# Kernel optimization log

Hardware: AMD Instinct MI355X
Metric: run time of the kernel (lower is better)

Reference implementation:

```python
import jax, jax.numpy as jnp
import numpy as np

D_MODEL = 1024
N_HEADS = 16
SCALES = (1, 2, 4, 8)
B, S = 4, 2048
NS = len(SCALES)
E = D_MODEL // NS        # per-scale embed dim = 256
H = N_HEADS // NS        # per-scale heads = 4
DK = E // H              # head dim = 64


def setup_inputs() -> dict:
    key = jax.random.key(0)
    ks = jax.random.split(key, 6)
    sc = lambda fan_in: 1.0 / np.sqrt(fan_in)
    return {
        "x": jax.random.normal(ks[0], (B, S, D_MODEL), jnp.float32),
        # per-scale projection Linear(d_model -> E), stacked over scales
        "proj_W": jax.random.normal(ks[1], (NS, D_MODEL, E), jnp.float32) * sc(D_MODEL),
        "proj_b": jnp.zeros((NS, E), jnp.float32),
        # per-scale MultiheadAttention in_proj (q,k,v packed) and out_proj
        "in_W": jax.random.normal(ks[2], (NS, E, 3 * E), jnp.float32) * sc(E),
        "in_b": jnp.zeros((NS, 3 * E), jnp.float32),
        "out_W": jax.random.normal(ks[3], (NS, E, E), jnp.float32) * sc(E),
        "out_b": jnp.zeros((NS, E), jnp.float32),
        # fusion: Linear(d_model -> d_model) + LayerNorm (dropout is identity in eval)
        "fus_W": jax.random.normal(ks[4], (D_MODEL, D_MODEL), jnp.float32) * sc(D_MODEL),
        "fus_b": jnp.zeros((D_MODEL,), jnp.float32),
        "ln_g": jnp.ones((D_MODEL,), jnp.float32),
        "ln_b": jnp.zeros((D_MODEL,), jnp.float32),
    }


def _mha(x, in_W, in_b, out_W, out_b):
    # torch nn.MultiheadAttention, batch_first, eval mode, need_weights=True
    b, L, _ = x.shape
    qkv = x @ in_W + in_b                       # [b, L, 3E]
    q, k, v = jnp.split(qkv, 3, axis=-1)
    heads = lambda t: t.reshape(b, L, H, DK).transpose(0, 2, 1, 3)  # [b,h,L,dk]
    q, k, v = heads(q), heads(k), heads(v)
    scores = jnp.einsum('bhqd,bhkd->bhqk', q, k) / np.sqrt(DK).astype(np.float32)
    probs = jax.nn.softmax(scores, axis=-1)
    o = jnp.einsum('bhqk,bhkd->bhqd', probs, v).transpose(0, 2, 1, 3).reshape(b, L, E)
    return o @ out_W + out_b, probs.mean(axis=1)  # averaged over heads: [b,L,L]


def _upsample(y, s):
    # Faithful vectorization of the torch interpolation loop when S % s == 0:
    # full[k*s + j] = (1 - j/s)*y[k] + (j/s)*y[k+1], with zero right-neighbor
    # for the last block (torch reads attn_out_full[S-1] while it is still 0).
    if s == 1:
        return y
    b, K, d = y.shape
    y_next = jnp.concatenate([y[:, 1:], jnp.zeros_like(y[:, :1])], axis=1)
    alpha = (jnp.arange(s, dtype=y.dtype) / s)[None, None, :, None]  # [1,1,s,1]
    full = (1.0 - alpha) * y[:, :, None, :] + alpha * y_next[:, :, None, :]
    return full.reshape(b, K * s, d)


def reference(x, proj_W, proj_b, in_W, in_b, out_W, out_b, fus_W, fus_b, ln_g, ln_b):
    scale_outputs = []
    w0 = None
    for i, s in enumerate(SCALES):
        x_scale = x @ proj_W[i] + proj_b[i]        # [B,S,E]
        x_sub = x_scale[:, ::s, :]                 # strided subsequence [B,S//s,E]
        y, w = _mha(x_sub, in_W[i], in_b[i], out_W[i], out_b[i])
        scale_outputs.append(_upsample(y, s))
        if i == 0:
            w0 = w                                  # combined_weights = first scale's weights
    z = jnp.concatenate(scale_outputs, axis=-1) @ fus_W + fus_b
    mu = z.mean(-1, keepdims=True)
    var = z.var(-1, keepdims=True)
    fused = (z - mu) / jnp.sqrt(var + 1e-5) * ln_g + ln_b
    return fused, w0
```

## Files before the change

kernel.cpp:

```cpp
#include <hip/hip_runtime.h>
#include <hip/hip_bf16.h>


typedef short bh8 __attribute__((ext_vector_type(8)));
typedef float f32x4 __attribute__((ext_vector_type(4)));

#define CLOG2E 0.18033688011112042f

__device__ __forceinline__ ushort f2b(float f) {
    __hip_bfloat16 h = __float2bfloat16(f);
    return *reinterpret_cast<ushort*>(&h);
}
__device__ __forceinline__ float b2f(ushort u) {
    __hip_bfloat16 h;
    *reinterpret_cast<ushort*>(&h) = u;
    return __bfloat162float(h);
}
__device__ __forceinline__ float fexp2(float x) {
    float r;
    asm("v_exp_f32 %0, %1" : "=v"(r) : "v"(x));
    return r;
}
template<int CTRL>
__device__ __forceinline__ float dpp_mv(float x) {
    int i = __float_as_int(x);
    int r = __builtin_amdgcn_update_dpp(i, i, CTRL, 0xF, 0xF, false);
    return __int_as_float(r);
}
__device__ __forceinline__ float row_max16(float t) {
    t = fmaxf(t, dpp_mv<0x128>(t));
    t = fmaxf(t, dpp_mv<0x124>(t));
    t = fmaxf(t, dpp_mv<0x122>(t));
    t = fmaxf(t, dpp_mv<0x121>(t));
    return t;
}
__device__ __forceinline__ float row_sum16(float t) {
    t += dpp_mv<0x128>(t);
    t += dpp_mv<0x124>(t);
    t += dpp_mv<0x122>(t);
    t += dpp_mv<0x121>(t);
    return t;
}

__global__ __launch_bounds__(256) void cvt_kernel(
    const float* __restrict__ s, ushort* __restrict__ d, long n)
{
    long i = ((long)blockIdx.x * 256 + threadIdx.x) * 4;
    if (i >= n) return;
    float4 v = *(const float4*)(s + i);
    ushort4 o;
    o.x = f2b(v.x); o.y = f2b(v.y); o.z = f2b(v.z); o.w = f2b(v.w);
    *(ushort4*)(d + i) = o;
}

__global__ __launch_bounds__(256) void wtrans_kernel(
    const float* __restrict__ src, ushort* __restrict__ dst, int K, int N)
{
    __shared__ float Ls[32][33];
    const int n0 = blockIdx.x * 32, k0 = blockIdx.y * 32;
    const float* s = src + (long)blockIdx.z * K * N;
    ushort* d = dst + (long)blockIdx.z * N * K;
    const int tid = threadIdx.x;
    #pragma unroll
    for (int it = 0; it < 4; ++it) {
        int f = tid + it * 256;
        int kc = f >> 5, rn = f & 31;
        Ls[kc][rn] = s[(long)(k0 + kc) * N + n0 + rn];
    }
    __syncthreads();
    #pragma unroll
    for (int it = 0; it < 2; ++it) {
        int f = tid + it * 256;
        int rn = f >> 4, kc2 = (f & 15) * 2;
        ushort2 o;
        o.x = f2b(Ls[kc2][rn]);
        o.y = f2b(Ls[kc2 + 1][rn]);
        *(ushort2*)&d[(long)(n0 + rn) * K + k0 + kc2] = o;
    }
}

template<int MODE>
__global__ __launch_bounds__(256) void gemm_ms(
    const ushort* __restrict__ A, const ushort* __restrict__ Wt,
    const float* __restrict__ bias, ushort* __restrict__ C)
{
    constexpr int K = (MODE == 0) ? 1024 : 256;
    constexpr int N = (MODE == 1) ? 768 : 256;
    __shared__ ushort As[128][72];
    __shared__ ushort Bs[128][72];

    const int tid = threadIdx.x;
    const int wave = tid >> 6, lane = tid & 63;
    const int lm = lane & 15, quad = lane >> 4;
    const int wm = (wave & 1) * 64, wn = (wave >> 1) * 64;
    const int m0 = blockIdx.x * 128, n0 = blockIdx.y * 128;
    const int s = (m0 >= 14336) ? 3 : ((m0 >= 12288) ? 2 : ((m0 >= 8192) ? 1 : 0));
    const ushort* Wp = Wt + (long)s * N * K;
    const float* bp_ = bias + s * N;

    f32x4 acc[4][4];
    #pragma unroll
    for (int i = 0; i < 4; ++i)
        #pragma unroll
        for (int j = 0; j < 4; ++j) {
            f32x4 zz = {0.f, 0.f, 0.f, 0.f};
            acc[i][j] = zz;
        }

    const int r0 = tid >> 3, k8 = (tid & 7) * 8;
    const ushort* ap[4];
    #pragma unroll
    for (int it = 0; it < 4; ++it) {
        int m = m0 + r0 + it * 32;
        if (MODE == 0) {
            int t = m - (16384 - (16384 >> s));
            int b = t >> (11 - s);
            int tt = t - (b << (11 - s));
            ap[it] = A + ((long)(b * 2048) + ((long)tt << s)) * 1024 + k8;
        } else {
            ap[it] = A + (long)m * K + k8;
        }
    }
    const ushort* bp[4];
    #pragma unroll
    for (int it = 0; it < 4; ++it)
        bp[it] = Wp + (long)(n0 + r0 + it * 32) * K + k8;

    for (int k0 = 0; k0 < K; k0 += 64) {
        #pragma unroll
        for (int it = 0; it < 4; ++it)
            *(bh8*)&As[r0 + it * 32][k8] = *(const bh8*)(ap[it] + k0);
        #pragma unroll
        for (int it = 0; it < 4; ++it)
            *(bh8*)&Bs[r0 + it * 32][k8] = *(const bh8*)(bp[it] + k0);
        __syncthreads();
        #pragma unroll
        for (int ks = 0; ks < 2; ++ks) {
            bh8 af[4], bfv[4];
            #pragma unroll
            for (int i = 0; i < 4; ++i)
                af[i] = *(const bh8*)&As[wm + i * 16 + lm][ks * 32 + quad * 8];
            #pragma unroll
            for (int j = 0; j < 4; ++j)
                bfv[j] = *(const bh8*)&Bs[wn + j * 16 + lm][ks * 32 + quad * 8];
            #pragma unroll
            for (int i = 0; i < 4; ++i)
                #pragma unroll
                for (int j = 0; j < 4; ++j)
                    acc[i][j] = __builtin_amdgcn_mfma_f32_16x16x32_bf16(
                        af[i], bfv[j], acc[i][j], 0, 0, 0);
        }
        __syncthreads();
    }

    float bv[4]; int cols[4];
    #pragma unroll
    for (int j = 0; j < 4; ++j) {
        cols[j] = n0 + wn + j * 16 + lm;
        bv[j] = bp_[cols[j]];
    }
    #pragma unroll
    for (int i = 0; i < 4; ++i) {
        int mb = m0 + wm + i * 16 + quad * 4;
        #pragma unroll
        for (int j = 0; j < 4; ++j)
            #pragma unroll
            for (int r = 0; r < 4; ++r)
                C[(long)(mb + r) * N + cols[j]] = f2b(acc[i][j][r] + bv[j]);
    }
}

__global__ __launch_bounds__(256) void vtrans_ms(
    const ushort* __restrict__ qkvb, ushort* __restrict__ vTb)
{
    __shared__ ushort Ls[64][72];
    const int bid = blockIdx.x;
    const int s = (bid >= 896) ? 3 : ((bid >= 768) ? 2 : ((bid >= 512) ? 1 : 0));
    const int rel = bid - ((s == 0) ? 0 : ((s == 1) ? 512 : ((s == 2) ? 768 : 896)));
    const int L = 2048 >> s;
    const int z = rel >> (5 - s);
    const int kt = rel & ((32 >> s) - 1);
    const int b = z >> 2, h = z & 3;
    const ushort* src = qkvb + (long)(16384 - (16384 >> s)) * 768
                        + (long)b * L * 768 + 512 + h * 64;
    const int k0 = kt * 64;
    const int tid = threadIdx.x;
    const int kk = tid >> 3, d8 = (tid & 7) * 8;
    #pragma unroll
    for (int it = 0; it < 2; ++it) {
        int k = kk + it * 32;
        bh8 v = *(const bh8*)(src + (long)(k0 + k) * 768 + d8);
        ushort tmp[8];
        *(bh8*)tmp = v;
        #pragma unroll
        for (int j = 0; j < 8; ++j) Ls[d8 + j][k] = tmp[j];
    }
    __syncthreads();
    ushort* dst = vTb + (long)(4096 - (4096 >> s)) * 1024 + (long)z * 64 * L;
    #pragma unroll
    for (int it = 0; it < 2; ++it) {
        int d = kk + it * 32;
        *(bh8*)(dst + (long)d * L + k0 + d8) = *(const bh8*)&Ls[d][d8];
    }
}

__global__ __launch_bounds__(256, 4) void attn_ms(
    const ushort* __restrict__ qkvb, const ushort* __restrict__ vTb,
    ushort* __restrict__ ob, float* __restrict__ msc, float* __restrict__ invl)
{
    __shared__ ushort KPs[128 * 72];
    __shared__ ushort Vs[64 * 136];

    const int bid = blockIdx.x;
    const int s = (bid >= 896) ? 3 : ((bid >= 768) ? 2 : ((bid >= 512) ? 1 : 0));
    const int rel = bid - ((s == 0) ? 0 : ((s == 1) ? 512 : ((s == 2) ? 768 : 896)));
    const int L = 2048 >> s;
    const int z = rel >> (5 - s);
    const int qt = rel & ((32 >> s) - 1);
    const int b = z >> 2, h = z & 3;
    const int Rr16 = 16384 - (16384 >> s);
    const ushort* qbase = qkvb + (long)Rr16 * 768 + (long)b * L * 768 + h * 64;
    const ushort* kbase = qbase + 256;
    const ushort* vbase = vTb + (long)(4096 - (4096 >> s)) * 1024 + (long)z * 64 * L;
    ushort* o = ob + (long)Rr16 * 256;

    const int tid = threadIdx.x;
    const int wave = tid >> 6, lane = tid & 63;
    const int lm = lane & 15, quad = lane >> 4;
    const int wm = wave * 16;
    const int q0 = qt * 64;
    const int r0 = tid >> 3, k8 = (tid & 7) * 8;
    const int vd0 = tid >> 4, vc8 = (tid & 15) * 8;

    #pragma unroll
    for (int it = 0; it < 2; ++it) {
        int row = r0 + it * 32;
        *(bh8*)&KPs[row * 72 + k8] = *(const bh8*)(qbase + (long)(q0 + row) * 768 + k8);
    }
    __syncthreads();
    bh8 qf[2];
    #pragma unroll
    for (int ks = 0; ks < 2; ++ks)
        qf[ks] = *(const bh8*)&KPs[(wm + lm) * 72 + ks * 32 + quad * 8];
    __syncthreads();

    f32x4 oc[4];
    #pragma unroll
    for (int nj = 0; nj < 4; ++nj) {
        f32x4 zz = {0.f, 0.f, 0.f, 0.f};
        oc[nj] = zz;
    }
    float mh[4], l_run[4];
    #pragma unroll
    for (int rr = 0; rr < 4; ++rr) { mh[rr] = -3.0e38f; l_run[rr] = 0.f; }

    for (int k0 = 0; k0 < L; k0 += 128) {
        #pragma unroll
        for (int it = 0; it < 4; ++it) {
            int row = r0 + it * 32;
            *(bh8*)&KPs[row * 72 + k8] = *(const bh8*)(kbase + (long)(k0 + row) * 768 + k8);
        }
        #pragma unroll
        for (int it = 0; it < 4; ++it) {
            int d = vd0 + it * 16;
            *(bh8*)&Vs[d * 136 + vc8] = *(const bh8*)(vbase + (long)d * L + k0 + vc8);
        }
        __syncthreads();

        f32x4 sc[8];
        #pragma unroll
        for (int nj = 0; nj < 8; ++nj) {
            f32x4 zz = {0.f, 0.f, 0.f, 0.f};
            sc[nj] = zz;
        }
        #pragma unroll
        for (int ks = 0; ks < 2; ++ks)
            #pragma unroll
            for (int nj = 0; nj < 8; ++nj) {
                bh8 kf = *(const bh8*)&KPs[(nj * 16 + lm) * 72 + ks * 32 + quad * 8];
                sc[nj] = __builtin_amdgcn_mfma_f32_16x16x32_bf16(qf[ks], kf, sc[nj], 0, 0, 0);
            }
        __syncthreads();

        #pragma unroll
        for (int rr = 0; rr < 4; ++rr) {
            float t01 = fmaxf(sc[0][rr], sc[1][rr]);
            float t23 = fmaxf(sc[2][rr], sc[3][rr]);
            float t45 = fmaxf(sc[4][rr], sc[5][rr]);
            float t67 = fmaxf(sc[6][rr], sc[7][rr]);
            float t = fmaxf(fmaxf(t01, t23), fmaxf(t45, t67));
            t = row_max16(t);
            float mo = mh[rr];
            float mn = fmaxf(mo, t * CLOG2E);
            float alpha = fexp2(mo - mn);
            mh[rr] = mn;
            int prow = (wm + quad * 4 + rr) * 136;
            float p[8];
            #pragma unroll
            for (int nj = 0; nj < 8; ++nj) {
                p[nj] = fexp2(fmaf(sc[nj][rr], CLOG2E, -mn));
                KPs[prow + nj * 16 + lm] = f2b(p[nj]);
            }
            float rs = ((p[0] + p[1]) + (p[2] + p[3])) + ((p[4] + p[5]) + (p[6] + p[7]));
            rs = row_sum16(rs);
            l_run[rr] = l_run[rr] * alpha + rs;
            #pragma unroll
            for (int nj = 0; nj < 4; ++nj) oc[nj][rr] *= alpha;
        }

        #pragma unroll
        for (int kst = 0; kst < 4; ++kst) {
            bh8 pf = *(const bh8*)&KPs[(wm + lm) * 136 + kst * 32 + quad * 8];
            #pragma unroll
            for (int nj = 0; nj < 4; ++nj) {
                bh8 vf = *(const bh8*)&Vs[(nj * 16 + lm) * 136 + kst * 32 + quad * 8];
                oc[nj] = __builtin_amdgcn_mfma_f32_16x16x32_bf16(pf, vf, oc[nj], 0, 0, 0);
            }
        }
        __syncthreads();
    }

    #pragma unroll
    for (int rr = 0; rr < 4; ++rr) {
        float il = 1.f / l_run[rr];
        int q = q0 + wm + quad * 4 + rr;
        if (s == 0 && lm == 0) {
            msc[z * 2048 + q] = mh[rr];
            invl[z * 2048 + q] = il;
        }
        long rbase = ((long)(b * L + q)) * 256 + h * 64;
        #pragma unroll
        for (int nj = 0; nj < 4; ++nj)
            o[rbase + nj * 16 + lm] = f2b(oc[nj][rr] * il);
    }
}

__global__ __launch_bounds__(256, 2) void w0_recompute(
    const ushort* __restrict__ qkv,
    const float* __restrict__ msc, const float* __restrict__ invl,
    float* __restrict__ w0)
{
    const int L = 2048;
    __shared__ ushort SH[18432];
    ushort* Qs = SH;
    ushort* Ks = SH + 9216;
    ushort* Ws = SH;

    const int tid = threadIdx.x;
    const int wave = tid >> 6, lane = tid & 63;
    const int lm = lane & 15, quad = lane >> 4;
    const int wm = wave * 32;
    const int q0 = blockIdx.x * 128, k0 = blockIdx.y * 128;
    const int b = blockIdx.z;
    const int r0 = tid >> 3, k8 = (tid & 7) * 8;

    f32x4 acc[2][8];
    #pragma unroll
    for (int mi = 0; mi < 2; ++mi)
        #pragma unroll
        for (int nj = 0; nj < 8; ++nj) {
            f32x4 zz = {0.f, 0.f, 0.f, 0.f};
            acc[mi][nj] = zz;
        }

    for (int h = 0; h < 4; ++h) {
        const ushort* qb = qkv + (long)b * L * 768 + h * 64;
        const ushort* kb = qb + 256;
        #pragma unroll
        for (int it = 0; it < 4; ++it) {
            int r = r0 + it * 32;
            *(bh8*)&Qs[r * 72 + k8] = *(const bh8*)(qb + (long)(q0 + r) * 768 + k8);
            *(bh8*)&Ks[r * 72 + k8] = *(const bh8*)(kb + (long)(k0 + r) * 768 + k8);
        }
        __syncthreads();
        bh8 qf[2][2];
        #pragma unroll
        for (int mi = 0; mi < 2; ++mi)
            #pragma unroll
            for (int ks = 0; ks < 2; ++ks)
                qf[mi][ks] = *(const bh8*)&Qs[(wm + mi * 16 + lm) * 72 + ks * 32 + quad * 8];
        f32x4 sc[2][8];
        #pragma unroll
        for (int mi = 0; mi < 2; ++mi)
            #pragma unroll
            for (int nj = 0; nj < 8; ++nj) {
                f32x4 zz = {0.f, 0.f, 0.f, 0.f};
                sc[mi][nj] = zz;
            }
        #pragma unroll
        for (int ks = 0; ks < 2; ++ks)
            #pragma unroll
            for (int nj = 0; nj < 8; ++nj) {
                bh8 kf = *(const bh8*)&Ks[(nj * 16 + lm) * 72 + ks * 32 + quad * 8];
                #pragma unroll
                for (int mi = 0; mi < 2; ++mi)
                    sc[mi][nj] = __builtin_amdgcn_mfma_f32_16x16x32_bf16(
                        qf[mi][ks], kf, sc[mi][nj], 0, 0, 0);
            }
        const float* mz = msc + (long)(b * 4 + h) * L;
        const float* iz = invl + (long)(b * 4 + h) * L;
        #pragma unroll
        for (int mi = 0; mi < 2; ++mi)
            #pragma unroll
            for (int rr = 0; rr < 4; ++rr) {
                int q = q0 + wm + mi * 16 + quad * 4 + rr;
                float mv = mz[q], iv = iz[q];
                #pragma unroll
                for (int nj = 0; nj < 8; ++nj)
                    acc[mi][nj][rr] += fexp2(fmaf(sc[mi][nj][rr], CLOG2E, -mv)) * iv;
            }
        __syncthreads();
    }

    #pragma unroll
    for (int mi = 0; mi < 2; ++mi)
        #pragma unroll
        for (int rr = 0; rr < 4; ++rr) {
            int prow = (wm + mi * 16 + quad * 4 + rr) * 136;
            #pragma unroll
            for (int nj = 0; nj < 8; ++nj)
                Ws[prow + nj * 16 + lm] = f2b(0.25f * acc[mi][nj][rr]);
        }
    __syncthreads();
    #pragma unroll
    for (int it = 0; it < 8; ++it) {
        int idx = tid + it * 256;
        int row = idx >> 4, c8 = (idx & 15) * 8;
        ushort tmp[8];
        *(bh8*)tmp = *(const bh8*)&Ws[row * 136 + c8];
        long base = ((long)b * 2048 + q0 + row) * 2048 + k0 + c8;
        float4 f0, f1;
        f0.x = b2f(tmp[0]); f0.y = b2f(tmp[1]); f0.z = b2f(tmp[2]); f0.w = b2f(tmp[3]);
        f1.x = b2f(tmp[4]); f1.y = b2f(tmp[5]); f1.z = b2f(tmp[6]); f1.w = b2f(tmp[7]);
        *(float4*)&w0[base] = f0;
        *(float4*)&w0[base + 4] = f1;
    }
}

__global__ __launch_bounds__(256) void upsample_ms(
    const ushort* __restrict__ yallb, ushort* __restrict__ ccat)
{
    const int bid = blockIdx.x;
    const int s = bid >> 11;
    const int idx = (bid & 2047) * 256 + threadIdx.x;
    const int c4 = (idx & 63) * 4;
    const int t = (idx >> 6) & 2047;
    const int b = idx >> 17;
    const int L = 2048 >> s;
    const int k = t >> s, j = t & ((1 << s) - 1);
    const float a = (float)j / (float)(1 << s);
    const ushort* y = yallb + (long)(16384 - (16384 >> s)) * 256;
    const ushort* y0p = y + ((long)(b * L + k)) * 256 + c4;
    ushort4 y0 = *(const ushort4*)y0p;
    ushort4 y1 = {0, 0, 0, 0};
    if (k + 1 < L) y1 = *(const ushort4*)(y0p + 256);
    ushort4 o;
    o.x = f2b((1.f - a) * b2f(y0.x) + a * b2f(y1.x));
    o.y = f2b((1.f - a) * b2f(y0.y) + a * b2f(y1.y));
    o.z = f2b((1.f - a) * b2f(y0.z) + a * b2f(y1.z));
    o.w = f2b((1.f - a) * b2f(y0.w) + a * b2f(y1.w));
    *(ushort4*)&ccat[((long)(b * 2048 + t)) * 1024 + s * 256 + c4] = o;
}

__global__ __launch_bounds__(256) void gemm_fus(
    const ushort* __restrict__ A, const ushort* __restrict__ Wt,
    const float* __restrict__ bias, float* __restrict__ C)
{
    const int K = 1024, N = 1024;
    __shared__ ushort As[128][72];
    __shared__ ushort Bs[128][72];
    const int tid = threadIdx.x;
    const int wave = tid >> 6, lane = tid & 63;
    const int lm = lane & 15, quad = lane >> 4;
    const int wm = (wave & 1) * 64, wn = (wave >> 1) * 64;
    const int m0 = blockIdx.x * 128, n0 = blockIdx.y * 128;

    f32x4 acc[4][4];
    #pragma unroll
    for (int i = 0; i < 4; ++i)
        #pragma unroll
        for (int j = 0; j < 4; ++j) {
            f32x4 zz = {0.f, 0.f, 0.f, 0.f};
            acc[i][j] = zz;
        }
    const int r0 = tid >> 3, k8 = (tid & 7) * 8;
    for (int k0 = 0; k0 < K; k0 += 64) {
        #pragma unroll
        for (int it = 0; it < 4; ++it) {
            int r = r0 + it * 32;
            *(bh8*)&As[r][k8] = *(const bh8*)(A + (long)(m0 + r) * K + k0 + k8);
            *(bh8*)&Bs[r][k8] = *(const bh8*)(Wt + (long)(n0 + r) * K + k0 + k8);
        }
        __syncthreads();
        #pragma unroll
        for (int ks = 0; ks < 2; ++ks) {
            bh8 af[4], bfv[4];
            #pragma unroll
            for (int i = 0; i < 4; ++i)
                af[i] = *(const bh8*)&As[wm + i * 16 + lm][ks * 32 + quad * 8];
            #pragma unroll
            for (int j = 0; j < 4; ++j)
                bfv[j] = *(const bh8*)&Bs[wn + j * 16 + lm][ks * 32 + quad * 8];
            #pragma unroll
            for (int i = 0; i < 4; ++i)
                #pragma unroll
                for (int j = 0; j < 4; ++j)
                    acc[i][j] = __builtin_amdgcn_mfma_f32_16x16x32_bf16(
                        af[i], bfv[j], acc[i][j], 0, 0, 0);
        }
        __syncthreads();
    }
    float bv[4]; int cols[4];
    #pragma unroll
    for (int j = 0; j < 4; ++j) {
        cols[j] = n0 + wn + j * 16 + lm;
        bv[j] = bias[cols[j]];
    }
    #pragma unroll
    for (int i = 0; i < 4; ++i) {
        int mb = m0 + wm + i * 16 + quad * 4;
        #pragma unroll
        for (int j = 0; j < 4; ++j)
            #pragma unroll
            for (int r = 0; r < 4; ++r)
                C[(long)(mb + r) * N + cols[j]] = acc[i][j][r] + bv[j];
    }
}

__global__ __launch_bounds__(256) void ln_kernel(
    float* __restrict__ zbuf, const float* __restrict__ g, const float* __restrict__ bta)
{
    long row = blockIdx.x;
    float* p = zbuf + row * 1024;
    const int tid = threadIdx.x;
    float4 v = *(const float4*)(p + tid * 4);
    float s = (v.x + v.y) + (v.z + v.w);
    #pragma unroll
    for (int off = 32; off; off >>= 1) s += __shfl_xor(s, off);
    __shared__ float r0[4], r1[4];
    int wid = tid >> 6;
    if ((tid & 63) == 0) r0[wid] = s;
    __syncthreads();
    s = r0[0] + r0[1] + r0[2] + r0[3];
    float mu = s * (1.f / 1024.f);
    float dx = v.x - mu, dy = v.y - mu, dz = v.z - mu, dw = v.w - mu;
    float q = (dx * dx + dy * dy) + (dz * dz + dw * dw);
    #pragma unroll
    for (int off = 32; off; off >>= 1) q += __shfl_xor(q, off);
    if ((tid & 63) == 0) r1[wid] = q;
    __syncthreads();
    q = r1[0] + r1[1] + r1[2] + r1[3];
    float rstd = rsqrtf(q * (1.f / 1024.f) + 1e-5f);
    float4 gg = *(const float4*)(g + tid * 4);
    float4 bb = *(const float4*)(bta + tid * 4);
    float4 o;
    o.x = dx * rstd * gg.x + bb.x;
    o.y = dy * rstd * gg.y + bb.y;
    o.z = dz * rstd * gg.z + bb.z;
    o.w = dw * rstd * gg.w + bb.w;
    *(float4*)(p + tid * 4) = o;
}

extern "C" void kernel_launch(void* const* d_in, const int* in_sizes, int n_in,
                              void* d_out, int out_size, void* d_ws, size_t ws_size,
                              hipStream_t stream)
{
    const float* x     = (const float*)d_in[0];
    const float* projW = (const float*)d_in[1];
    const float* projB = (const float*)d_in[2];
    const float* inW   = (const float*)d_in[3];
    const float* inB   = (const float*)d_in[4];
    const float* outW  = (const float*)d_in[5];
    const float* outB  = (const float*)d_in[6];
    const float* fusW  = (const float*)d_in[7];
    const float* fusB  = (const float*)d_in[8];
    const float* lnG   = (const float*)d_in[9];
    const float* lnB   = (const float*)d_in[10];

    float* fused  = (float*)d_out;
    float* out_w0 = fused + 8388608;

    char* w = (char*)d_ws;
    ushort* xb     = (ushort*)w; w += 16777216;
    ushort* pT     = (ushort*)w; w += 2097152;
    ushort* iT     = (ushort*)w; w += 1572864;
    ushort* oT     = (ushort*)w; w += 524288;
    ushort* fT     = (ushort*)w; w += 2097152;
    ushort* xprojb = (ushort*)w; w += 7864320;
    ushort* qkvb   = (ushort*)w; w += 23592960;
    ushort* ob     = (ushort*)w; w += 7864320;
    ushort* yallb  = (ushort*)w; w += 7864320;
    ushort* ccatb  = (ushort*)w; w += 16777216;
    ushort* vTb    = (ushort*)w; w += 7864320;
    float*  msc    = (float*)w;  w += 131072;
    float*  invl   = (float*)w;  w += 131072;

    cvt_kernel<<<8192, 256, 0, stream>>>(x, xb, 8388608);
    wtrans_kernel<<<dim3(8, 32, 4), 256, 0, stream>>>(projW, pT, 1024, 256);
    wtrans_kernel<<<dim3(24, 8, 4), 256, 0, stream>>>(inW, iT, 256, 768);
    wtrans_kernel<<<dim3(8, 8, 4), 256, 0, stream>>>(outW, oT, 256, 256);
    wtrans_kernel<<<dim3(32, 32, 1), 256, 0, stream>>>(fusW, fT, 1024, 1024);

    gemm_ms<0><<<dim3(120, 2), 256, 0, stream>>>(xb, pT, projB, xprojb);
    gemm_ms<1><<<dim3(120, 6), 256, 0, stream>>>(xprojb, iT, inB, qkvb);
    vtrans_ms<<<960, 256, 0, stream>>>(qkvb, vTb);
    attn_ms<<<960, 256, 0, stream>>>(qkvb, vTb, ob, msc, invl);
    w0_recompute<<<dim3(16, 16, 4), 256, 0, stream>>>(qkvb, msc, invl, out_w0);
    gemm_ms<2><<<dim3(120, 2), 256, 0, stream>>>(ob, oT, outB, yallb);
    upsample_ms<<<8192, 256, 0, stream>>>(yallb, ccatb);
    gemm_fus<<<dim3(64, 8), 256, 0, stream>>>(ccatb, fT, fusB, fused);
    ln_kernel<<<8192, 256, 0, stream>>>(fused, lnG, lnB);
}
```

Before: 358.5 us.

## Split scale-0 attention over key chunks and merge partials in a combine kernel

Scale-0 attention blocks, which previously walked all 2048 keys, are split into four 512-key chunks. Each chunk writes unnormalized fp32 partial outputs plus the running max and sum into reused workspace. A new combine kernel merges the four partials with log-sum-exp weights and writes the bf16 output along with the max and inverse-sum needed by w0_recompute. The probability tile also gets its own shared buffer, which drops two barriers, at the cost of more LDS per block and lower occupancy. The goal is to shorten the long scale-0 critical path and balance work across CUs, in exchange for extra fp32 partial traffic and one more kernel launch.

New measurement: 365.1 us. About the same (+1.8%).

```diff
diff --git a/kernel.cpp b/kernel.cpp
--- a/kernel.cpp
+++ b/kernel.cpp
@@ -204,25 +204,29 @@
     }
 }
 
-__global__ __launch_bounds__(256, 4) void attn_ms(
+__global__ __launch_bounds__(256, 3) void attn_ms(
     const ushort* __restrict__ qkvb, const ushort* __restrict__ vTb,
-    ushort* __restrict__ ob, float* __restrict__ msc, float* __restrict__ invl)
-{
-    __shared__ ushort KPs[128 * 72];
+    ushort* __restrict__ ob, float* __restrict__ opB, float* __restrict__ opA,
+    float* __restrict__ mlb)
+{
+    __shared__ ushort Ks[128 * 72];
     __shared__ ushort Vs[64 * 136];
+    __shared__ ushort Ps[64 * 136];
 
     const int bid = blockIdx.x;
-    const int s = (bid >= 896) ? 3 : ((bid >= 768) ? 2 : ((bid >= 512) ? 1 : 0));
-    const int rel = bid - ((s == 0) ? 0 : ((s == 1) ? 512 : ((s == 2) ? 768 : 896)));
+    int s, c, z, qt;
+    if (bid < 2048)      { s = 0; c = bid >> 9; int r = bid & 511; z = r >> 5; qt = r & 31; }
+    else if (bid < 2304) { s = 1; c = 0; int r = bid - 2048; z = r >> 4; qt = r & 15; }
+    else if (bid < 2432) { s = 2; c = 0; int r = bid - 2304; z = r >> 3; qt = r & 7; }
+    else                 { s = 3; c = 0; int r = bid - 2432; z = r >> 2; qt = r & 3; }
     const int L = 2048 >> s;
-    const int z = rel >> (5 - s);
-    const int qt = rel & ((32 >> s) - 1);
+    const int kbeg = c << 9;
+    const int kend = (s == 0) ? (kbeg + 512) : L;
     const int b = z >> 2, h = z & 3;
     const int Rr16 = 16384 - (16384 >> s);
     const ushort* qbase = qkvb + (long)Rr16 * 768 + (long)b * L * 768 + h * 64;
     const ushort* kbase = qbase + 256;
     const ushort* vbase = vTb + (long)(4096 - (4096 >> s)) * 1024 + (long)z * 64 * L;
-    ushort* o = ob + (long)Rr16 * 256;
 
     const int tid = threadIdx.x;
     const int wave = tid >> 6, lane = tid & 63;
@@ -235,14 +239,13 @@
     #pragma unroll
     for (int it = 0; it < 2; ++it) {
         int row = r0 + it * 32;
-        *(bh8*)&KPs[row * 72 + k8] = *(const bh8*)(qbase + (long)(q0 + row) * 768 + k8);
+        *(bh8*)&Ps[row * 136 + k8] = *(const bh8*)(qbase + (long)(q0 + row) * 768 + k8);
     }
     __syncthreads();
     bh8 qf[2];
     #pragma unroll
     for (int ks = 0; ks < 2; ++ks)
-        qf[ks] = *(const bh8*)&KPs[(wm + lm) * 72 + ks * 32 + quad * 8];
-    __syncthreads();
+        qf[ks] = *(const bh8*)&Ps[(wm + lm) * 136 + ks * 32 + quad * 8];
 
     f32x4 oc[4];
     #pragma unroll
@@ -254,11 +257,11 @@
     #pragma unroll
     for (int rr = 0; rr < 4; ++rr) { mh[rr] = -3.0e38f; l_run[rr] = 0.f; }
 
-    for (int k0 = 0; k0 < L; k0 += 128) {
+    for (int k0 = kbeg; k0 < kend; k0 += 128) {
         #pragma unroll
         for (int it = 0; it < 4; ++it) {
             int row = r0 + it * 32;
-            *(bh8*)&KPs[row * 72 + k8] = *(const bh8*)(kbase + (long)(k0 + row) * 768 + k8);
+            *(bh8*)&Ks[row * 72 + k8] = *(const bh8*)(kbase + (long)(k0 + row) * 768 + k8);
         }
         #pragma unroll
         for (int it = 0; it < 4; ++it) {
@@ -277,10 +280,9 @@
         for (int ks = 0; ks < 2; ++ks)
             #pragma unroll
             for (int nj = 0; nj < 8; ++nj) {
-                bh8 kf = *(const bh8*)&KPs[(nj * 16 + lm) * 72 + ks * 32 + quad * 8];
+                bh8 kf = *(const bh8*)&Ks[(nj * 16 + lm) * 72 + ks * 32 + quad * 8];
                 sc[nj] = __builtin_amdgcn_mfma_f32_16x16x32_bf16(qf[ks], kf, sc[nj], 0, 0, 0);
             }
-        __syncthreads();
 
         #pragma unroll
         for (int rr = 0; rr < 4; ++rr) {
@@ -299,7 +301,7 @@
             #pragma unroll
             for (int nj = 0; nj < 8; ++nj) {
                 p[nj] = fexp2(fmaf(sc[nj][rr], CLOG2E, -mn));
-                KPs[prow + nj * 16 + lm] = f2b(p[nj]);
+                Ps[prow + nj * 16 + lm] = f2b(p[nj]);
             }
             float rs = ((p[0] + p[1]) + (p[2] + p[3])) + ((p[4] + p[5]) + (p[6] + p[7]));
             rs = row_sum16(rs);
@@ -310,7 +312,7 @@
 
         #pragma unroll
         for (int kst = 0; kst < 4; ++kst) {
-            bh8 pf = *(const bh8*)&KPs[(wm + lm) * 136 + kst * 32 + quad * 8];
+            bh8 pf = *(const bh8*)&Ps[(wm + lm) * 136 + kst * 32 + quad * 8];
             #pragma unroll
             for (int nj = 0; nj < 4; ++nj) {
                 bh8 vf = *(const bh8*)&Vs[(nj * 16 + lm) * 136 + kst * 32 + quad * 8];
@@ -320,19 +322,60 @@
         __syncthreads();
     }
 
-    #pragma unroll
-    for (int rr = 0; rr < 4; ++rr) {
-        float il = 1.f / l_run[rr];
-        int q = q0 + wm + quad * 4 + rr;
-        if (s == 0 && lm == 0) {
-            msc[z * 2048 + q] = mh[rr];
-            invl[z * 2048 + q] = il;
-        }
-        long rbase = ((long)(b * L + q)) * 256 + h * 64;
-        #pragma unroll
-        for (int nj = 0; nj < 4; ++nj)
-            o[rbase + nj * 16 + lm] = f2b(oc[nj][rr] * il);
-    }
+    if (s == 0) {
+        float* op = (c < 2) ? (opB + (long)c * 2097152) : (opA + (long)(c - 2) * 2097152);
+        float2* ml = (float2*)mlb;
+        #pragma unroll
+        for (int rr = 0; rr < 4; ++rr) {
+            int q = q0 + wm + quad * 4 + rr;
+            int row = z * 2048 + q;
+            if (lm == 0) {
+                float2 v = {mh[rr], l_run[rr]};
+                ml[c * 32768 + row] = v;
+            }
+            long rbase = (long)row * 64;
+            #pragma unroll
+            for (int nj = 0; nj < 4; ++nj)
+                op[rbase + nj * 16 + lm] = oc[nj][rr];
+        }
+    } else {
+        ushort* o = ob + (long)Rr16 * 256;
+        #pragma unroll
+        for (int rr = 0; rr < 4; ++rr) {
+            float il = 1.f / l_run[rr];
+            int q = q0 + wm + quad * 4 + rr;
+            long rbase = ((long)(b * L + q)) * 256 + h * 64;
+            #pragma unroll
+            for (int nj = 0; nj < 4; ++nj)
+                o[rbase + nj * 16 + lm] = f2b(oc[nj][rr] * il);
+        }
+    }
+}
+
+__global__ __launch_bounds__(256) void attn_combine(
+    const float* __restrict__ opB, const float* __restrict__ opA,
+    const float* __restrict__ mlb, ushort* __restrict__ ob,
+    float* __restrict__ msc, float* __restrict__ invl)
+{
+    const int gw = (blockIdx.x << 2) + (threadIdx.x >> 6);
+    const int lane = threadIdx.x & 63;
+    const float2* ml = (const float2*)mlb;
+    float2 ml0 = ml[gw];
+    float2 ml1 = ml[32768 + gw];
+    float2 ml2 = ml[65536 + gw];
+    float2 ml3 = ml[98304 + gw];
+    float M = fmaxf(fmaxf(ml0.x, ml1.x), fmaxf(ml2.x, ml3.x));
+    float w0_ = fexp2(ml0.x - M), w1 = fexp2(ml1.x - M);
+    float w2 = fexp2(ml2.x - M), w3 = fexp2(ml3.x - M);
+    float l = w0_ * ml0.y + w1 * ml1.y + w2 * ml2.y + w3 * ml3.y;
+    long rb = (long)gw * 64 + lane;
+    float o = w0_ * opB[rb] + w1 * opB[2097152 + rb]
+            + w2 * opA[rb] + w3 * opA[2097152 + rb];
+    float il = 1.f / l;
+    int z = gw >> 11, q = gw & 2047;
+    int b = z >> 2, h = z & 3;
+    ob[((long)(b * 2048 + q)) * 256 + h * 64 + lane] = f2b(o * il);
+    if (lane == 0) { msc[gw] = M; invl[gw] = il; }
 }
 
 __global__ __launch_bounds__(256, 2) void w0_recompute(
@@ -595,6 +638,10 @@
     float*  msc    = (float*)w;  w += 131072;
     float*  invl   = (float*)w;  w += 131072;
 
+    float* opA = (float*)d_ws;
+    float* opB = (float*)yallb;
+    float* mlb = (float*)((char*)yallb + 16777216);
+
     cvt_kernel<<<8192, 256, 0, stream>>>(x, xb, 8388608);
     wtrans_kernel<<<dim3(8, 32, 4), 256, 0, stream>>>(projW, pT, 1024, 256);
     wtrans_kernel<<<dim3(24, 8, 4), 256, 0, stream>>>(inW, iT, 256, 768);
@@ -604,7 +651,8 @@
     gemm_ms<0><<<dim3(120, 2), 256, 0, stream>>>(xb, pT, projB, xprojb);
     gemm_ms<1><<<dim3(120, 6), 256, 0, stream>>>(xprojb, iT, inB, qkvb);
     vtrans_ms<<<960, 256, 0, stream>>>(qkvb, vTb);
-    attn_ms<<<960, 256, 0, stream>>>(qkvb, vTb, ob, msc, invl);
+    attn_ms<<<2496, 256, 0, stream>>>(qkvb, vTb, ob, opB, opA, mlb);
+    attn_combine<<<8192, 256, 0, stream>>>(opB, opA, mlb, ob, msc, invl);
     w0_recompute<<<dim3(16, 16, 4), 256, 0, stream>>>(qkvb, msc, invl, out_w0);
     gemm_ms<2><<<dim3(120, 2), 256, 0, stream>>>(ob, oT, outB, yallb);
     upsample_ms<<<8192, 256, 0, stream>>>(yallb, ccatb);
```

## Prefetch next K/V tile into registers and split P buffer from K in attention

Applied to the files above, without the earlier changes.

The attention kernel now loads the next K and V tiles from global memory into registers while the current tile is being computed, and writes them to shared memory after the PV step. The probabilities get their own shared buffer instead of reusing the K buffer, which removes the barrier between QK and the P writes. MFMA sections are wrapped in s_setprio. The costs are more shared memory and register use, and launch bounds drop from 4 to 3 blocks per CU, so occupancy falls.

After: 340.1 us. 1.05x faster.

```diff
diff --git a/kernel.cpp b/kernel.cpp
--- a/kernel.cpp
+++ b/kernel.cpp
@@ -204,12 +204,13 @@
     }
 }
 
-__global__ __launch_bounds__(256, 4) void attn_ms(
+__global__ __launch_bounds__(256, 3) void attn_ms(
     const ushort* __restrict__ qkvb, const ushort* __restrict__ vTb,
     ushort* __restrict__ ob, float* __restrict__ msc, float* __restrict__ invl)
 {
-    __shared__ ushort KPs[128 * 72];
+    __shared__ ushort Ks[128 * 72];
     __shared__ ushort Vs[64 * 136];
+    __shared__ ushort Ps[64 * 136];
 
     const int bid = blockIdx.x;
     const int s = (bid >= 896) ? 3 : ((bid >= 768) ? 2 : ((bid >= 512) ? 1 : 0));
@@ -235,14 +236,27 @@
     #pragma unroll
     for (int it = 0; it < 2; ++it) {
         int row = r0 + it * 32;
-        *(bh8*)&KPs[row * 72 + k8] = *(const bh8*)(qbase + (long)(q0 + row) * 768 + k8);
-    }
+        *(bh8*)&Ps[row * 136 + k8] = *(const bh8*)(qbase + (long)(q0 + row) * 768 + k8);
+    }
+    bh8 kreg[4], vreg[4];
+    #pragma unroll
+    for (int it = 0; it < 4; ++it)
+        kreg[it] = *(const bh8*)(kbase + (long)(r0 + it * 32) * 768 + k8);
+    #pragma unroll
+    for (int it = 0; it < 4; ++it)
+        vreg[it] = *(const bh8*)(vbase + (long)(vd0 + it * 16) * L + vc8);
+    #pragma unroll
+    for (int it = 0; it < 4; ++it)
+        *(bh8*)&Ks[(r0 + it * 32) * 72 + k8] = kreg[it];
+    #pragma unroll
+    for (int it = 0; it < 4; ++it)
+        *(bh8*)&Vs[(vd0 + it * 16) * 136 + vc8] = vreg[it];
     __syncthreads();
+
     bh8 qf[2];
     #pragma unroll
     for (int ks = 0; ks < 2; ++ks)
-        qf[ks] = *(const bh8*)&KPs[(wm + lm) * 72 + ks * 32 + quad * 8];
-    __syncthreads();
+        qf[ks] = *(const bh8*)&Ps[(wm + lm) * 136 + ks * 32 + quad * 8];
 
     f32x4 oc[4];
     #pragma unroll
@@ -255,17 +269,16 @@
     for (int rr = 0; rr < 4; ++rr) { mh[rr] = -3.0e38f; l_run[rr] = 0.f; }
 
     for (int k0 = 0; k0 < L; k0 += 128) {
-        #pragma unroll
-        for (int it = 0; it < 4; ++it) {
-            int row = r0 + it * 32;
-            *(bh8*)&KPs[row * 72 + k8] = *(const bh8*)(kbase + (long)(k0 + row) * 768 + k8);
-        }
-        #pragma unroll
-        for (int it = 0; it < 4; ++it) {
-            int d = vd0 + it * 16;
-            *(bh8*)&Vs[d * 136 + vc8] = *(const bh8*)(vbase + (long)d * L + k0 + vc8);
-        }
-        __syncthreads();
+        const int kn = k0 + 128;
+        const bool hasnext = kn < L;
+        if (hasnext) {
+            #pragma unroll
+            for (int it = 0; it < 4; ++it)
+                kreg[it] = *(const bh8*)(kbase + (long)(kn + r0 + it * 32) * 768 + k8);
+            #pragma unroll
+            for (int it = 0; it < 4; ++it)
+                vreg[it] = *(const bh8*)(vbase + (long)(vd0 + it * 16) * L + kn + vc8);
+        }
 
         f32x4 sc[8];
         #pragma unroll
@@ -273,14 +286,15 @@
             f32x4 zz = {0.f, 0.f, 0.f, 0.f};
             sc[nj] = zz;
         }
+        __builtin_amdgcn_s_setprio(1);
         #pragma unroll
         for (int ks = 0; ks < 2; ++ks)
             #pragma unroll
             for (int nj = 0; nj < 8; ++nj) {
-                bh8 kf = *(const bh8*)&KPs[(nj * 16 + lm) * 72 + ks * 32 + quad * 8];
+                bh8 kf = *(const bh8*)&Ks[(nj * 16 + lm) * 72 + ks * 32 + quad * 8];
                 sc[nj] = __builtin_amdgcn_mfma_f32_16x16x32_bf16(qf[ks], kf, sc[nj], 0, 0, 0);
             }
-        __syncthreads();
+        __builtin_amdgcn_s_setprio(0);
 
         #pragma unroll
         for (int rr = 0; rr < 4; ++rr) {
@@ -299,7 +313,7 @@
             #pragma unroll
             for (int nj = 0; nj < 8; ++nj) {
                 p[nj] = fexp2(fmaf(sc[nj][rr], CLOG2E, -mn));
-                KPs[prow + nj * 16 + lm] = f2b(p[nj]);
+                Ps[prow + nj * 16 + lm] = f2b(p[nj]);
             }
             float rs = ((p[0] + p[1]) + (p[2] + p[3])) + ((p[4] + p[5]) + (p[6] + p[7]));
             rs = row_sum16(rs);
@@ -308,16 +322,28 @@
             for (int nj = 0; nj < 4; ++nj) oc[nj][rr] *= alpha;
         }
 
+        __builtin_amdgcn_s_setprio(1);
         #pragma unroll
         for (int kst = 0; kst < 4; ++kst) {
-            bh8 pf = *(const bh8*)&KPs[(wm + lm) * 136 + kst * 32 + quad * 8];
+            bh8 pf = *(const bh8*)&Ps[(wm + lm) * 136 + kst * 32 + quad * 8];
             #pragma unroll
             for (int nj = 0; nj < 4; ++nj) {
                 bh8 vf = *(const bh8*)&Vs[(nj * 16 + lm) * 136 + kst * 32 + quad * 8];
                 oc[nj] = __builtin_amdgcn_mfma_f32_16x16x32_bf16(pf, vf, oc[nj], 0, 0, 0);
             }
         }
+        __builtin_amdgcn_s_setprio(0);
+
         __syncthreads();
+        if (hasnext) {
+            #pragma unroll
+            for (int it = 0; it < 4; ++it)
+                *(bh8*)&Ks[(r0 + it * 32) * 72 + k8] = kreg[it];
+            #pragma unroll
+            for (int it = 0; it < 4; ++it)
+                *(bh8*)&Vs[(vd0 + it * 16) * 136 + vc8] = vreg[it];
+            __syncthreads();
+        }
     }
 
     #pragma unroll
```
